# Optimization experiments

Hardware: AMD Instinct MI355X
Metric: run time of the kernel (lower is better)

## Reference

```python
import jax, jax.numpy as jnp
import numpy as np

QMAX = 127.0

def _quantize_int8(x, axis):
    """Symmetric dynamic int8 quantization along `axis`. Returns (int8 values, fp32 scale)."""
    amax = jnp.max(jnp.abs(x), axis=axis, keepdims=True)
    scale = jnp.maximum(amax, 1e-8) / QMAX
    q = jnp.clip(jnp.round(x / scale), -QMAX, QMAX).astype(jnp.int8)
    return q, scale


def setup_inputs() -> dict:
    key = jax.random.key(0)
    kx, kw, kb = jax.random.split(key, 3)
    tokens, d_in, d_out = 4096, 4096, 16384
    x = jax.random.normal(kx, (tokens, d_in), dtype=jnp.float32)
    weight = jax.random.normal(kw, (d_out, d_in), dtype=jnp.float32) * (1.0 / np.sqrt(d_in))
    bias = jax.random.normal(kb, (d_out,), dtype=jnp.float32)
    return {"x": x, "weight": weight, "bias": bias}


def reference(x, weight, bias):
    # Quantize activations per-row (over in_features), weights per-output-column.
    xq, sx = _quantize_int8(x, axis=-1)            # [T, in] int8, [T, 1] scale
    wq, sw = _quantize_int8(weight.T, axis=0)      # [in, out] int8, [1, out] scale
    acc = jnp.matmul(xq, wq, preferred_element_type=jnp.int32)  # [T, out] int32
    out = acc.astype(jnp.float32) * sx * sw + bias
    return out
```

## Files before the change

### kernel.cpp

```cpp
#include <hip/hip_runtime.h>
#include <stdint.h>

typedef int   i32x4 __attribute__((ext_vector_type(4)));
typedef float f32x4 __attribute__((ext_vector_type(4)));

#define AS1 __attribute__((address_space(1)))
#define AS3 __attribute__((address_space(3)))
#define G2L16(gp, lp) __builtin_amdgcn_global_load_lds((const AS1 void*)(gp), (AS3 void*)(lp), 16, 0, 0)

template<int COLS>
__global__ __launch_bounds__(256)
void quant_rows_k(const float* __restrict__ src, int8_t* __restrict__ q,
                  float* __restrict__ scale)
{
    constexpr int PER = COLS / 256;
    static_assert(PER == 16, "pack assumes 16 elems/thread");
    const int row = blockIdx.x;
    const int t   = threadIdx.x;
    const float* s = src + (size_t)row * COLS + (size_t)t * PER;

    float v[PER];
    #pragma unroll
    for (int i = 0; i < PER; i += 4) {
        f32x4 x4 = *reinterpret_cast<const f32x4*>(s + i);
        v[i+0] = x4[0]; v[i+1] = x4[1]; v[i+2] = x4[2]; v[i+3] = x4[3];
    }
    float amax = 0.0f;
    #pragma unroll
    for (int i = 0; i < PER; ++i) amax = fmaxf(amax, fabsf(v[i]));

    #pragma unroll
    for (int off = 32; off > 0; off >>= 1)
        amax = fmaxf(amax, __shfl_xor(amax, off, 64));

    __shared__ float red[4];
    if ((t & 63) == 0) red[t >> 6] = amax;
    __syncthreads();
    amax = fmaxf(fmaxf(red[0], red[1]), fmaxf(red[2], red[3]));

    const float sc = fmaxf(amax, 1e-8f) / 127.0f;
    if (t == 0) scale[row] = sc;

    union { i32x4 v4; int8_t b[16]; } pk;
    #pragma unroll
    for (int i = 0; i < PER; ++i) {
        float r = rintf(v[i] / sc);
        r = fminf(127.0f, fmaxf(-127.0f, r));
        pk.b[i] = (int8_t)r;
    }
    *reinterpret_cast<i32x4*>(q + (size_t)row * COLS + (size_t)t * PER) = pk.v4;
}

#define BM 256
#define BN 256
#define BKB 128

__device__ __forceinline__ i32x4 mfma_i8(i32x4 a, i32x4 b, i32x4 c) {
    return __builtin_amdgcn_mfma_i32_16x16x64_i8(a, b, c, 0, 0, 0);
}

template<int P>
__device__ __forceinline__ void phase_fn(
    const int8_t* __restrict__ aB, const int8_t* __restrict__ bB,
    int kc0, int kc1,
    i32x4 (&acc)[8][4], i32x4 (&bf)[4][2],
    const int8_t* __restrict__ gSt, int8_t* lSt, size_t row64, int t16, bool doStage)
{
    i32x4 a00 = *reinterpret_cast<const i32x4*>(aB + (2*P)   * 2048 + kc0);
    i32x4 a01 = *reinterpret_cast<const i32x4*>(aB + (2*P)   * 2048 + kc1);
    i32x4 a10 = *reinterpret_cast<const i32x4*>(aB + (2*P+1) * 2048 + kc0);
    i32x4 a11 = *reinterpret_cast<const i32x4*>(aB + (2*P+1) * 2048 + kc1);
    if (P == 0) {
        #pragma unroll
        for (int ni = 0; ni < 4; ++ni) {
            bf[ni][0] = *reinterpret_cast<const i32x4*>(bB + ni * 2048 + kc0);
            bf[ni][1] = *reinterpret_cast<const i32x4*>(bB + ni * 2048 + kc1);
        }
    }
    if (doStage) {
        G2L16(gSt,         lSt + t16);
        G2L16(gSt + row64, lSt + 8192 + t16);
    }
    asm volatile("" ::: "memory");
    __builtin_amdgcn_s_barrier();
    asm volatile("s_waitcnt lgkmcnt(0)" ::: "memory");
    __builtin_amdgcn_sched_barrier(0);
    __builtin_amdgcn_s_setprio(1);
    #pragma unroll
    for (int ni = 0; ni < 4; ++ni) {
        acc[2*P  ][ni] = mfma_i8(a00, bf[ni][0], acc[2*P  ][ni]);
        acc[2*P  ][ni] = mfma_i8(a01, bf[ni][1], acc[2*P  ][ni]);
        acc[2*P+1][ni] = mfma_i8(a10, bf[ni][0], acc[2*P+1][ni]);
        acc[2*P+1][ni] = mfma_i8(a11, bf[ni][1], acc[2*P+1][ni]);
    }
    __builtin_amdgcn_s_setprio(0);
    asm volatile("" ::: "memory");
    __builtin_amdgcn_s_barrier();
}

__global__ __launch_bounds__(512, 2)
void gemm_i8_k(const int8_t* __restrict__ A,
               const int8_t* __restrict__ B,
               const float*  __restrict__ sx,
               const float*  __restrict__ sw,
               const float*  __restrict__ bias,
               float* __restrict__ C,
               int M, int N, int K)
{
    __shared__ int8_t lA[2][BM * BKB];
    __shared__ int8_t lB[2][BN * BKB];

    const int t    = threadIdx.x;
    const int lane = t & 63;
    const int wid  = t >> 6;
    const int wm   = wid >> 2;
    const int wn   = wid & 3;

    const int nwg = (int)gridDim.x;
    const int bid = (int)blockIdx.x;
    const int swz = ((nwg & 7) == 0) ? ((bid & 7) * (nwg >> 3) + (bid >> 3)) : bid;
    const int nbn = N / BN;
    const int bm  = swz / nbn;
    const int bn  = swz % nbn;

    const int fr  = lane & 15;
    const int c4  = lane >> 4;
    const int sw8 = fr & 7;
    const int kc0 = ((c4    ) ^ sw8) * 16;
    const int kc1 = ((c4 + 4) ^ sw8) * 16;
    const int8_t* aB0 = &lA[0][(wm * 128 + fr) * BKB];
    const int8_t* aB1 = &lA[1][(wm * 128 + fr) * BKB];
    const int8_t* bB0 = &lB[0][(wn * 64  + fr) * BKB];
    const int8_t* bB1 = &lB[1][(wn * 64  + fr) * BKB];

    const int srow = t >> 3;
    const int skc  = ((t & 7) ^ (srow & 7)) * 16;
    const int t16  = t * 16;
    const int8_t* pA = A + (size_t)(bm * BM + srow) * K + skc;
    const int8_t* pB = B + (size_t)(bn * BN + srow) * K + skc;
    const size_t row64  = (size_t)64  * K;
    const size_t row128 = (size_t)128 * K;

    G2L16(pA,                  &lA[0][0]     + t16);
    G2L16(pA + row64,          &lA[0][8192]  + t16);
    G2L16(pA + row128,         &lA[0][16384] + t16);
    G2L16(pA + row128 + row64, &lA[0][24576] + t16);
    G2L16(pB,                  &lB[0][0]     + t16);
    G2L16(pB + row64,          &lB[0][8192]  + t16);
    G2L16(pB + row128,         &lB[0][16384] + t16);
    G2L16(pB + row128 + row64, &lB[0][24576] + t16);

    i32x4 acc[8][4] = {};
    i32x4 bf[4][2];

    const int NT = K / BKB;
    for (int tt = 0; tt < NT; tt += 2) {
        {
            asm volatile("s_waitcnt vmcnt(0)" ::: "memory");
            __builtin_amdgcn_s_barrier();
            asm volatile("" ::: "memory");
            const size_t ko = (size_t)(tt + 1) * BKB;
            phase_fn<0>(aB0, bB0, kc0, kc1, acc, bf, pA + ko,          &lA[1][0],     row64, t16, true);
            phase_fn<1>(aB0, bB0, kc0, kc1, acc, bf, pA + row128 + ko, &lA[1][16384], row64, t16, true);
            phase_fn<2>(aB0, bB0, kc0, kc1, acc, bf, pB + ko,          &lB[1][0],     row64, t16, true);
            phase_fn<3>(aB0, bB0, kc0, kc1, acc, bf, pB + row128 + ko, &lB[1][16384], row64, t16, true);
        }
        {
            asm volatile("s_waitcnt vmcnt(0)" ::: "memory");
            __builtin_amdgcn_s_barrier();
            asm volatile("" ::: "memory");
            const bool st = (tt + 2) < NT;
            const size_t ko = st ? (size_t)(tt + 2) * BKB : 0;
            phase_fn<0>(aB1, bB1, kc0, kc1, acc, bf, pA + ko,          &lA[0][0],     row64, t16, st);
            phase_fn<1>(aB1, bB1, kc0, kc1, acc, bf, pA + row128 + ko, &lA[0][16384], row64, t16, st);
            phase_fn<2>(aB1, bB1, kc0, kc1, acc, bf, pB + ko,          &lB[0][0],     row64, t16, st);
            phase_fn<3>(aB1, bB1, kc0, kc1, acc, bf, pB + row128 + ko, &lB[0][16384], row64, t16, st);
        }
    }

    const int r0 = bm * BM + wm * 128 + (c4 << 2);
    const int c0 = bn * BN + wn * 64 + fr;
    #pragma unroll
    for (int ni = 0; ni < 4; ++ni) {
        const int c = c0 + ni * 16;
        const float swc = sw[c];
        const float bc  = bias[c];
        #pragma unroll
        for (int mi = 0; mi < 8; ++mi) {
            const int rb = r0 + mi * 16;
            #pragma unroll
            for (int j = 0; j < 4; ++j) {
                const int r = rb + j;
                C[(size_t)r * N + c] = (float)acc[mi][ni][j] * sx[r] * swc + bc;
            }
        }
    }
}

extern "C" void kernel_launch(void* const* d_in, const int* in_sizes, int n_in,
                              void* d_out, int out_size, void* d_ws, size_t ws_size,
                              hipStream_t stream) {
    const float* x    = (const float*)d_in[0];
    const float* w    = (const float*)d_in[1];
    const float* bias = (const float*)d_in[2];
    float* out = (float*)d_out;

    const int dout   = in_sizes[2];
    const int din    = in_sizes[1] / dout;
    const int tokens = in_sizes[0] / din;

    char* ws = (char*)d_ws;
    float*  sx = (float*)ws;
    float*  sw = (float*)(ws + 16384);
    int8_t* xq = (int8_t*)(ws + 16384 + 65536);
    int8_t* wq = xq + (size_t)tokens * din;

    quant_rows_k<4096><<<tokens, 256, 0, stream>>>(x, xq, sx);
    quant_rows_k<4096><<<dout,   256, 0, stream>>>(w, wq, sw);

    const int grid = (tokens / BM) * (dout / BN);
    gemm_i8_k<<<grid, 512, 0, stream>>>(xq, wq, sx, sw, bias, out, tokens, dout, din);
}
```

Before: 443.9 us.

## Reorder staged loads and use partial vmcnt waits to overlap prefetch with compute

Changes the order of the global-to-LDS prefetch so B tiles load first and A rows are interleaved. The full vmcnt(0) wait plus barrier at the start of each half-iteration is replaced by partial waits (vmcnt(4), vmcnt(2)) at the end of phases 1 and 3. The aim is to let the next tile's consumption begin while later loads are still in flight, cutting stall time at tile boundaries. The correctness of the partial waits depends on the exact issue order of the loads versus which LDS rows each phase reads.

```diff
diff --git a/kernel.cpp b/kernel.cpp
--- a/kernel.cpp
+++ b/kernel.cpp
@@ -59,12 +59,14 @@
     return __builtin_amdgcn_mfma_i32_16x16x64_i8(a, b, c, 0, 0, 0);
 }
 
-template<int P>
+template<int P, int WAIT>
 __device__ __forceinline__ void phase_fn(
     const int8_t* __restrict__ aB, const int8_t* __restrict__ bB,
     int kc0, int kc1,
     i32x4 (&acc)[8][4], i32x4 (&bf)[4][2],
-    const int8_t* __restrict__ gSt, int8_t* lSt, size_t row64, int t16, bool doStage)
+    const int8_t* __restrict__ g0, int8_t* l0,
+    const int8_t* __restrict__ g1, int8_t* l1,
+    int t16, bool doStage)
 {
     i32x4 a00 = *reinterpret_cast<const i32x4*>(aB + (2*P)   * 2048 + kc0);
     i32x4 a01 = *reinterpret_cast<const i32x4*>(aB + (2*P)   * 2048 + kc1);
@@ -78,8 +80,8 @@
         }
     }
     if (doStage) {
-        G2L16(gSt,         lSt + t16);
-        G2L16(gSt + row64, lSt + 8192 + t16);
+        G2L16(g0, l0 + t16);
+        G2L16(g1, l1 + t16);
     }
     asm volatile("" ::: "memory");
     __builtin_amdgcn_s_barrier();
@@ -94,8 +96,17 @@
         acc[2*P+1][ni] = mfma_i8(a11, bf[ni][1], acc[2*P+1][ni]);
     }
     __builtin_amdgcn_s_setprio(0);
+    if (WAIT >= 0) {
+        if (doStage) {
+            if (WAIT == 4) asm volatile("s_waitcnt vmcnt(4)" ::: "memory");
+            else           asm volatile("s_waitcnt vmcnt(2)" ::: "memory");
+        } else {
+            asm volatile("s_waitcnt vmcnt(0)" ::: "memory");
+        }
+    }
     asm volatile("" ::: "memory");
     __builtin_amdgcn_s_barrier();
+    asm volatile("" ::: "memory");
 }
 
 __global__ __launch_bounds__(512, 2)
@@ -138,17 +149,20 @@
     const int t16  = t * 16;
     const int8_t* pA = A + (size_t)(bm * BM + srow) * K + skc;
     const int8_t* pB = B + (size_t)(bn * BN + srow) * K + skc;
-    const size_t row64  = (size_t)64  * K;
-    const size_t row128 = (size_t)128 * K;
-
-    G2L16(pA,                  &lA[0][0]     + t16);
-    G2L16(pA + row64,          &lA[0][8192]  + t16);
-    G2L16(pA + row128,         &lA[0][16384] + t16);
-    G2L16(pA + row128 + row64, &lA[0][24576] + t16);
-    G2L16(pB,                  &lB[0][0]     + t16);
-    G2L16(pB + row64,          &lB[0][8192]  + t16);
-    G2L16(pB + row128,         &lB[0][16384] + t16);
-    G2L16(pB + row128 + row64, &lB[0][24576] + t16);
+    const size_t r64  = (size_t)64  * K;
+    const size_t r128 = (size_t)128 * K;
+
+    G2L16(pB,              &lB[0][0]     + t16);
+    G2L16(pB + r64,        &lB[0][8192]  + t16);
+    G2L16(pB + 2*r64,      &lB[0][16384] + t16);
+    G2L16(pB + 3*r64,      &lB[0][24576] + t16);
+    G2L16(pA,              &lA[0][0]     + t16);
+    G2L16(pA + r128,       &lA[0][16384] + t16);
+    G2L16(pA + r64,        &lA[0][8192]  + t16);
+    G2L16(pA + r128 + r64, &lA[0][24576] + t16);
+    asm volatile("s_waitcnt vmcnt(2)" ::: "memory");
+    __builtin_amdgcn_s_barrier();
+    asm volatile("" ::: "memory");
 
     i32x4 acc[8][4] = {};
     i32x4 bf[4][2];
@@ -156,25 +170,19 @@
     const int NT = K / BKB;
     for (int tt = 0; tt < NT; tt += 2) {
         {
-            asm volatile("s_waitcnt vmcnt(0)" ::: "memory");
-            __builtin_amdgcn_s_barrier();
-            asm volatile("" ::: "memory");
             const size_t ko = (size_t)(tt + 1) * BKB;
-            phase_fn<0>(aB0, bB0, kc0, kc1, acc, bf, pA + ko,          &lA[1][0],     row64, t16, true);
-            phase_fn<1>(aB0, bB0, kc0, kc1, acc, bf, pA + row128 + ko, &lA[1][16384], row64, t16, true);
-            phase_fn<2>(aB0, bB0, kc0, kc1, acc, bf, pB + ko,          &lB[1][0],     row64, t16, true);
-            phase_fn<3>(aB0, bB0, kc0, kc1, acc, bf, pB + row128 + ko, &lB[1][16384], row64, t16, true);
+            phase_fn<0,-1>(aB0, bB0, kc0, kc1, acc, bf, pB + ko,              &lB[1][0],     pB + ko + r64,        &lB[1][8192],  t16, true);
+            phase_fn<1, 4>(aB0, bB0, kc0, kc1, acc, bf, pB + ko + 2*r64,      &lB[1][16384], pB + ko + 3*r64,      &lB[1][24576], t16, true);
+            phase_fn<2,-1>(aB0, bB0, kc0, kc1, acc, bf, pA + ko,              &lA[1][0],     pA + ko + r128,       &lA[1][16384], t16, true);
+            phase_fn<3, 2>(aB0, bB0, kc0, kc1, acc, bf, pA + ko + r64,        &lA[1][8192],  pA + ko + r128 + r64, &lA[1][24576], t16, true);
         }
         {
-            asm volatile("s_waitcnt vmcnt(0)" ::: "memory");
-            __builtin_amdgcn_s_barrier();
-            asm volatile("" ::: "memory");
             const bool st = (tt + 2) < NT;
             const size_t ko = st ? (size_t)(tt + 2) * BKB : 0;
-            phase_fn<0>(aB1, bB1, kc0, kc1, acc, bf, pA + ko,          &lA[0][0],     row64, t16, st);
-            phase_fn<1>(aB1, bB1, kc0, kc1, acc, bf, pA + row128 + ko, &lA[0][16384], row64, t16, st);
-            phase_fn<2>(aB1, bB1, kc0, kc1, acc, bf, pB + ko,          &lB[0][0],     row64, t16, st);
-            phase_fn<3>(aB1, bB1, kc0, kc1, acc, bf, pB + row128 + ko, &lB[0][16384], row64, t16, st);
+            phase_fn<0,-1>(aB1, bB1, kc0, kc1, acc, bf, pB + ko,              &lB[0][0],     pB + ko + r64,        &lB[0][8192],  t16, st);
+            phase_fn<1, 4>(aB1, bB1, kc0, kc1, acc, bf, pB + ko + 2*r64,      &lB[0][16384], pB + ko + 3*r64,      &lB[0][24576], t16, st);
+            phase_fn<2,-1>(aB1, bB1, kc0, kc1, acc, bf, pA + ko,              &lA[0][0],     pA + ko + r128,       &lA[0][16384], t16, st);
+            phase_fn<3, 2>(aB1, bB1, kc0, kc1, acc, bf, pA + ko + r64,        &lA[0][8192],  pA + ko + r128 + r64, &lA[0][24576], t16, st);
         }
     }
 
```

Measured after the change: 422.8 us. 4.8% less time.
